# Kernel optimization log

Measured on AMD Instinct MI355X. Metric: run time of the kernel, lower is better.

## Reference

```python
import jax, jax.numpy as jnp
import numpy as np

B, S, H, OUT, L = 32, 4096, 128, 128, 3


def _log_g(x):
    return jnp.where(x >= 0, jnp.log(jax.nn.relu(x) + 0.5), -jax.nn.softplus(-x))


def _cell(x, Wz, bz, Wh, bh):
    # x: [B, S, Din] -> h: [B, S, H]
    k = x @ Wz.T + bz                              # [B,S,H]
    log_z = -jax.nn.softplus(-k)
    log_coeffs = -jax.nn.softplus(k)
    # h_0 = zeros -> log_g(0) = log(0.5)
    log_h0 = jnp.full((x.shape[0], 1, k.shape[-1]), np.log(0.5), dtype=k.dtype)
    log_tilde_h = _log_g(x @ Wh.T + bh)
    log_values = jnp.concatenate([log_h0, log_z + log_tilde_h], axis=1)  # [B,S+1,H]
    # FAITHFUL to source: cumsum over the FEATURE axis (dim=-1), pad along seq
    a_star = jnp.pad(jnp.cumsum(log_coeffs, axis=-1), ((0, 0), (1, 0), (0, 0)))
    log_h = a_star + jax.lax.cumlogsumexp(log_values - a_star, axis=1)
    # torch forward applies sigmoid to the cell output, then drops the h_0 row
    return jax.nn.sigmoid(jnp.exp(log_h))[:, 1:, :]


def setup_inputs() -> dict:
    key = jax.random.key(0)
    ks = jax.random.split(key, 2 * L + 2)
    inp = {"x": jax.random.normal(ks[0], (B, S), dtype=jnp.float32)}
    for l in range(L):
        din = 1 if l == 0 else H
        inp[f"Wz{l}"] = jax.random.normal(ks[1 + 2 * l], (H, din), dtype=jnp.float32) * 0.02
        inp[f"bz{l}"] = jnp.zeros((H,), dtype=jnp.float32)
        inp[f"Wh{l}"] = jax.random.normal(ks[2 + 2 * l], (H, din), dtype=jnp.float32) * 0.02
        inp[f"bh{l}"] = jnp.zeros((H,), dtype=jnp.float32)
    inp["Wout"] = jax.random.normal(ks[-1], (OUT, H * S), dtype=jnp.float32) * (1.0 / np.sqrt(H * S))
    inp["bout"] = jnp.zeros((OUT,), dtype=jnp.float32)
    return inp


def reference(x, Wz0, bz0, Wh0, bh0, Wz1, bz1, Wh1, bh1, Wz2, bz2, Wh2, bh2, Wout, bout):
    h = x[:, :, None]  # [B,S,1]
    for (Wz, bz, Wh, bh) in ((Wz0, bz0, Wh0, bh0), (Wz1, bz1, Wh1, bh1), (Wz2, bz2, Wh2, bh2)):
        h = _cell(h, Wz, bz, Wh, bh)
    flat = h.reshape(h.shape[0], -1)  # [B, S*H]
    return flat @ Wout.T + bout       # [B, OUT]
```

## Files before the change

kernel.cpp:

```cpp
#include <hip/hip_runtime.h>
#include <hip/hip_bf16.h>
#include <math.h>

#define B_   32
#define S_   4096
#define H_   128
#define OUT_ 128
#define P_   (B_*S_)
#define NC_  64
#define CH_  (S_/NC_)
#define NKS_ 512
#define KTOT_ (H_*S_)
#define NEGINF_ (-__builtin_inff())
#define HTP_ 136
#define LOGHALF_ (-0.6931471805599453f)

typedef __bf16 bf16x8 __attribute__((ext_vector_type(8)));
typedef float  f32x4  __attribute__((ext_vector_type(4)));
typedef unsigned short ushort8_t __attribute__((ext_vector_type(8)));

__device__ __forceinline__ float sp_(float x) {
  return __logf(1.f + __expf(x));
}
__device__ __forceinline__ float logg_(float x) {
  float t = (x >= 0.f) ? (x + 0.5f) : __builtin_amdgcn_rcpf(1.f + __expf(-x));
  return __logf(t);
}
__device__ __forceinline__ float lae_(float a, float b) {
  float m = fmaxf(a, b);
  float d = -fabsf(a - b);
  return m + __logf(1.f + __expf(d));
}
__device__ __forceinline__ float sigm_(float e) {
  return __builtin_amdgcn_rcpf(1.f + __expf(-e));
}
__device__ __forceinline__ unsigned short f2bf_(float f) {
  unsigned int u = __float_as_uint(f);
  u += 0x7fffu + ((u >> 16) & 1u);
  return (unsigned short)(u >> 16);
}

#define DPPADD_(v, ctrl, rmask) \
  ((v) + __int_as_float(__builtin_amdgcn_update_dpp( \
      0, __float_as_int(v), (ctrl), (rmask), 0xf, true)))
__device__ __forceinline__ float wscan_(float v) {
  v = DPPADD_(v, 0x111, 0xf);
  v = DPPADD_(v, 0x112, 0xf);
  v = DPPADD_(v, 0x114, 0xf);
  v = DPPADD_(v, 0x118, 0xf);
  v = DPPADD_(v, 0x142, 0xa);
  v = DPPADD_(v, 0x143, 0xc);
  return v;
}


__global__ __launch_bounds__(256) void prep0c_kernel(
    const float* __restrict__ x,
    const float* __restrict__ Wz, const float* __restrict__ bz,
    const float* __restrict__ Wh, const float* __restrict__ bh,
    float* __restrict__ ua, float* __restrict__ tot,
    const float* __restrict__ Wz1, const float* __restrict__ Wh1,
    const float* __restrict__ Wz2, const float* __restrict__ Wh2,
    unsigned short* __restrict__ Wc1, unsigned short* __restrict__ Wc2)
{
  __shared__ float tpart[4][128];
  if (blockIdx.x >= 2048) {
    int idx = (blockIdx.x - 2048) * 256 + threadIdx.x;
    Wc1[idx] = f2bf_(idx < 16384 ? Wz1[idx] : Wh1[idx - 16384]);
    Wc2[idx] = f2bf_(idx < 16384 ? Wz2[idx] : Wh2[idx - 16384]);
    return;
  }
  int lane = threadIdx.x & 63, w = threadIdx.x >> 6;
  float wz0 = Wz[lane], wz1 = Wz[lane + 64];
  float bz0 = bz[lane], bz1 = bz[lane + 64];
  float wh0 = Wh[lane], wh1 = Wh[lane + 64];
  float bh0 = bh[lane], bh1 = bh[lane + 64];
  int blk = blockIdx.x;
  size_t base2 = (size_t)blk * (CH_ * 256);
  int pos0 = blk * CH_;
  float xv[16];
  #pragma unroll
  for (int j = 0; j < 16; ++j) xv[j] = x[pos0 + j * 4 + w];
  float t0 = NEGINF_, t1 = NEGINF_;
  #pragma unroll
  for (int j = 0; j < 16; ++j) {
    int i = j * 4 + w;
    float k0 = fmaf(xv[j], wz0, bz0), k1 = fmaf(xv[j], wz1, bz1);
    float g0 = fmaf(xv[j], wh0, bh0), g1 = fmaf(xv[j], wh1, bh1);
    float lc0 = -sp_(k0), lc1 = -sp_(k1);
    float lv0 = k0 + lc0 + logg_(g0);
    float lv1 = k1 + lc1 + logg_(g1);
    float s0 = wscan_(lc0);
    float c0 = __shfl(s0, 63, 64);
    float s1 = wscan_(lc1) + c0;
    float u0 = lv0 - s0, u1 = lv1 - s1;
    size_t o2 = base2 + (size_t)i * 256;
    *reinterpret_cast<float2*>(&ua[o2 + 2 * lane])       = make_float2(u0, s0);
    *reinterpret_cast<float2*>(&ua[o2 + 128 + 2 * lane]) = make_float2(u1, s1);
    t0 = lae_(t0, u0); t1 = lae_(t1, u1);
  }
  tpart[w][lane] = t0; tpart[w][64 + lane] = t1;
  __syncthreads();
  if (w == 0) {
    int ch = lane;
    tot[(size_t)blk * H_ + ch] =
        lae_(lae_(tpart[0][ch], tpart[1][ch]), lae_(tpart[2][ch], tpart[3][ch]));
    ch = lane + 64;
    tot[(size_t)blk * H_ + ch] =
        lae_(lae_(tpart[0][ch], tpart[1][ch]), lae_(tpart[2][ch], tpart[3][ch]));
  }
}

__global__ __launch_bounds__(256) void kb_kernel(
    const float* __restrict__ totIn,
    const unsigned short* __restrict__ Wc,
    const float* __restrict__ bz, const float* __restrict__ bh,
    float* __restrict__ ua,
    float* __restrict__ totOut)
{
  __shared__ unsigned short hT[64][HTP_];
  __shared__ union {
    float kg[16][260];
    float scr[32][128];
  } ks;
  __shared__ float thand[128];
  __shared__ float tpart[4][128];
  int tid = threadIdx.x;
  int lane = tid & 63, w = tid >> 6;
  int l15 = lane & 15, quad = lane >> 4;
  int half = tid >> 7, ch = tid & 127;
  int blk = blockIdx.x;
  int cidx = blk & (NC_ - 1);
  size_t base2 = (size_t)blk * (CH_ * 256);

  {
    const float* tp = totIn + (size_t)(blk - cidx) * H_ + ch;
    float p0 = NEGINF_, p1 = NEGINF_;
    int i = half;
    for (; i + 2 < cidx; i += 4) {
      float a0 = tp[(size_t)i * H_];
      float a1 = tp[(size_t)(i + 2) * H_];
      p0 = lae_(p0, a0); p1 = lae_(p1, a1);
    }
    for (; i < cidx; i += 2) p0 = lae_(p0, tp[(size_t)i * H_]);
    tpart[half * 2][ch] = p0; tpart[half * 2 + 1][ch] = p1;
  }
  __syncthreads();

  const float* stp = ua + base2 + 2 * ch;

  if (half == 0) {
    float r = LOGHALF_;
    r = lae_(r, tpart[0][ch]); r = lae_(r, tpart[1][ch]);
    r = lae_(r, tpart[2][ch]); r = lae_(r, tpart[3][ch]);
    float uv[32], av[32];
    #pragma unroll
    for (int i = 0; i < 32; ++i) {
      float2 v = *reinterpret_cast<const float2*>(stp + (size_t)i * 256);
      uv[i] = v.x; av[i] = v.y;
    }
    #pragma unroll
    for (int i = 0; i < 32; ++i) {
      r = lae_(r, uv[i]);
      hT[i][ch] = f2bf_(sigm_(__expf(av[i] + r)));
    }
    thand[ch] = r;
  } else {
    float r = NEGINF_;
    float uv[32];
    #pragma unroll
    for (int i = 0; i < 32; ++i)
      uv[i] = stp[(size_t)(32 + i) * 256];
    #pragma unroll
    for (int i = 0; i < 32; ++i) { r = lae_(r, uv[i]); ks.scr[i][ch] = r; }
  }
  __syncthreads();
  if (half == 1) {
    float r31 = thand[ch];
    float av[32];
    #pragma unroll
    for (int i = 0; i < 32; ++i) av[i] = stp[(size_t)(32 + i) * 256 + 1];
    #pragma unroll
    for (int i = 0; i < 32; ++i) {
      float ri = lae_(r31, ks.scr[i][ch]);
      hT[32 + i][ch] = f2bf_(sigm_(__expf(av[i] + ri)));
    }
  }
  __syncthreads();

  float bz0v = bz[lane], bz1v = bz[lane + 64];
  float bh0v = bh[lane], bh1v = bh[lane + 64];
  float t0 = NEGINF_, t1 = NEGINF_;

  for (int t = 0; t < 4; ++t) {
    f32x4 z = {0.f, 0.f, 0.f, 0.f};
    f32x4 acc[4] = {z, z, z, z};
    #pragma unroll
    for (int kk = 0; kk < 4; ++kk) {
      bf16x8 a = *reinterpret_cast<const bf16x8*>(&hT[t * 16 + l15][kk * 32 + quad * 8]);
      #pragma unroll
      for (int nt = 0; nt < 4; ++nt) {
        int n = w * 64 + nt * 16 + l15;
        bf16x8 bf = *reinterpret_cast<const bf16x8*>(Wc + n * 128 + kk * 32 + quad * 8);
        acc[nt] = __builtin_amdgcn_mfma_f32_16x16x32_bf16(a, bf, acc[nt], 0, 0, 0);
      }
    }
    __syncthreads();
    #pragma unroll
    for (int nt = 0; nt < 4; ++nt) {
      int col = w * 64 + nt * 16 + l15;
      #pragma unroll
      for (int r2 = 0; r2 < 4; ++r2)
        ks.kg[quad * 4 + r2][col] = acc[nt][r2];
    }
    __syncthreads();
    #pragma unroll
    for (int i = 0; i < 4; ++i) {
      int row = w + i * 4;
      int sIdx = t * 16 + row;
      float k0 = ks.kg[row][lane]        + bz0v;
      float k1 = ks.kg[row][64 + lane]   + bz1v;
      float g0 = ks.kg[row][128 + lane]  + bh0v;
      float g1 = ks.kg[row][192 + lane]  + bh1v;
      float lc0 = -sp_(k0), lc1 = -sp_(k1);
      float lv0 = k0 + lc0 + logg_(g0);
      float lv1 = k1 + lc1 + logg_(g1);
      float s0 = wscan_(lc0);
      float c0 = __shfl(s0, 63, 64);
      float s1 = wscan_(lc1) + c0;
      float u0 = lv0 - s0, u1 = lv1 - s1;
      size_t o2 = base2 + (size_t)sIdx * 256;
      *reinterpret_cast<float2*>(&ua[o2 + 2 * lane])       = make_float2(u0, s0);
      *reinterpret_cast<float2*>(&ua[o2 + 128 + 2 * lane]) = make_float2(u1, s1);
      t0 = lae_(t0, u0); t1 = lae_(t1, u1);
    }
  }

  tpart[w][lane] = t0; tpart[w][64 + lane] = t1;
  __syncthreads();
  if (w == 0) {
    int c = lane;
    totOut[(size_t)blk * H_ + c] =
        lae_(lae_(tpart[0][c], tpart[1][c]), lae_(tpart[2][c], tpart[3][c]));
    c = lane + 64;
    totOut[(size_t)blk * H_ + c] =
        lae_(lae_(tpart[0][c], tpart[1][c]), lae_(tpart[2][c], tpart[3][c]));
  }
}

__global__ __launch_bounds__(256) void scan3v2_kernel(
    const float* __restrict__ ua,
    const float* __restrict__ totIn, unsigned short* __restrict__ hbf)
{
  __shared__ float scr[32][128];
  __shared__ float thand[128];
  __shared__ float tpart[4][128];
  int tid = threadIdx.x;
  int half = tid >> 7, ch = tid & 127;
  int blk = blockIdx.x;
  int cidx = blk & (NC_ - 1);
  size_t base2 = (size_t)blk * (CH_ * 256);
  size_t baseh = (size_t)blk * (CH_ * H_);
  const float* stp = ua + base2 + 2 * ch;
  unsigned short* hp = hbf + baseh + ch;

  {
    const float* tp = totIn + (size_t)(blk - cidx) * H_ + ch;
    float p0 = NEGINF_, p1 = NEGINF_;
    int i = half;
    for (; i + 2 < cidx; i += 4) {
      float a0 = tp[(size_t)i * H_];
      float a1 = tp[(size_t)(i + 2) * H_];
      p0 = lae_(p0, a0); p1 = lae_(p1, a1);
    }
    for (; i < cidx; i += 2) p0 = lae_(p0, tp[(size_t)i * H_]);
    tpart[half * 2][ch] = p0; tpart[half * 2 + 1][ch] = p1;
  }
  __syncthreads();

  if (half == 0) {
    float r = LOGHALF_;
    r = lae_(r, tpart[0][ch]); r = lae_(r, tpart[1][ch]);
    r = lae_(r, tpart[2][ch]); r = lae_(r, tpart[3][ch]);
    float uv[32], av[32];
    #pragma unroll
    for (int i = 0; i < 32; ++i) {
      float2 v = *reinterpret_cast<const float2*>(stp + (size_t)i * 256);
      uv[i] = v.x; av[i] = v.y;
    }
    #pragma unroll
    for (int i = 0; i < 32; ++i) {
      r = lae_(r, uv[i]);
      hp[(size_t)i * H_] = f2bf_(sigm_(__expf(av[i] + r)));
    }
    thand[ch] = r;
  } else {
    float r = NEGINF_;
    float uv[32];
    #pragma unroll
    for (int i = 0; i < 32; ++i) uv[i] = stp[(size_t)(32 + i) * 256];
    #pragma unroll
    for (int i = 0; i < 32; ++i) { r = lae_(r, uv[i]); scr[i][ch] = r; }
  }
  __syncthreads();
  if (half == 1) {
    float r31 = thand[ch];
    float av[32];
    #pragma unroll
    for (int i = 0; i < 32; ++i) av[i] = stp[(size_t)(32 + i) * 256 + 1];
    #pragma unroll
    for (int i = 0; i < 32; ++i) {
      float ri = lae_(r31, scr[i][ch]);
      hp[(size_t)(32 + i) * H_] = f2bf_(sigm_(__expf(av[i] + ri)));
    }
  }
}

__device__ __forceinline__ void omload_(
    const unsigned short* ap0, const unsigned short* ap1,
    const float* wp0, const float* wp1, int k,
    bf16x8& a0r, bf16x8& a1r, float4 (&wr)[2][2])
{
  a0r = *reinterpret_cast<const bf16x8*>(ap0 + k);
  a1r = *reinterpret_cast<const bf16x8*>(ap1 + k);
  wr[0][0] = *reinterpret_cast<const float4*>(wp0 + k);
  wr[0][1] = *reinterpret_cast<const float4*>(wp0 + k + 4);
  wr[1][0] = *reinterpret_cast<const float4*>(wp1 + k);
  wr[1][1] = *reinterpret_cast<const float4*>(wp1 + k + 4);
}
__device__ __forceinline__ void omstep_(
    const bf16x8& a0r, const bf16x8& a1r,
    const float4 (&wr)[2][2], f32x4 (&acc)[2][2])
{
  #pragma unroll
  for (int nt = 0; nt < 2; ++nt) {
    ushort8_t tt;
    tt[0] = f2bf_(wr[nt][0].x); tt[1] = f2bf_(wr[nt][0].y);
    tt[2] = f2bf_(wr[nt][0].z); tt[3] = f2bf_(wr[nt][0].w);
    tt[4] = f2bf_(wr[nt][1].x); tt[5] = f2bf_(wr[nt][1].y);
    tt[6] = f2bf_(wr[nt][1].z); tt[7] = f2bf_(wr[nt][1].w);
    bf16x8 bf = __builtin_bit_cast(bf16x8, tt);
    acc[0][nt] = __builtin_amdgcn_mfma_f32_16x16x32_bf16(a0r, bf, acc[0][nt], 0, 0, 0);
    acc[1][nt] = __builtin_amdgcn_mfma_f32_16x16x32_bf16(a1r, bf, acc[1][nt], 0, 0, 0);
  }
}

__global__ __launch_bounds__(256) void outmm_kernel(
    const unsigned short* __restrict__ hbf,
    const float* __restrict__ Wout,
    float* __restrict__ part)
{
  const int KSL = KTOT_ / NKS_;
  int tid = threadIdx.x, w = tid >> 6, lane = tid & 63;
  int l15 = lane & 15, quad = lane >> 4;
  int k0base = blockIdx.x * KSL;
  const unsigned short* ap0 = hbf + (size_t)l15 * KTOT_ + k0base + quad * 8;
  const unsigned short* ap1 = hbf + (size_t)(16 + l15) * KTOT_ + k0base + quad * 8;
  const float* wp0 = Wout + (size_t)(w * 32 + l15) * KTOT_ + k0base + quad * 8;
  const float* wp1 = Wout + (size_t)(w * 32 + 16 + l15) * KTOT_ + k0base + quad * 8;
  f32x4 acc[2][2] = {{{0,0,0,0},{0,0,0,0}},{{0,0,0,0},{0,0,0,0}}};
  bf16x8 aA0, aA1, aB0, aB1;
  float4 wvA[2][2], wvB[2][2];
  omload_(ap0, ap1, wp0, wp1, 0, aA0, aA1, wvA);
  for (int ks = 0; ks < KSL; ks += 64) {
    omload_(ap0, ap1, wp0, wp1, ks + 32, aB0, aB1, wvB);
    omstep_(aA0, aA1, wvA, acc);
    if (ks + 64 < KSL) omload_(ap0, ap1, wp0, wp1, ks + 64, aA0, aA1, wvA);
    omstep_(aB0, aB1, wvB, acc);
  }
  float* pp = part + (size_t)blockIdx.x * (B_ * OUT_);
  #pragma unroll
  for (int mt = 0; mt < 2; ++mt)
    #pragma unroll
    for (int nt = 0; nt < 2; ++nt)
      #pragma unroll
      for (int r = 0; r < 4; ++r) {
        int b = mt * 16 + quad * 4 + r;
        int o = w * 32 + nt * 16 + l15;
        pp[b * OUT_ + o] = acc[mt][nt][r];
      }
}

__global__ __launch_bounds__(256) void outred_kernel(
    const float* __restrict__ part, const float* __restrict__ bout,
    float* __restrict__ out)
{
  __shared__ float red[4][64];
  int w = threadIdx.x >> 6, lane = threadIdx.x & 63;
  int idx0 = blockIdx.x * 64;
  float s = 0.f;
  for (int wg = w; wg < NKS_; wg += 4)
    s += part[(size_t)wg * (B_ * OUT_) + idx0 + lane];
  red[w][lane] = s;
  __syncthreads();
  if (w == 0) {
    float r = (red[0][lane] + red[1][lane]) + (red[2][lane] + red[3][lane]);
    int idx = idx0 + lane;
    out[idx] = r + bout[idx & (OUT_ - 1)];
  }
}

extern "C" void kernel_launch(void* const* d_in, const int* in_sizes, int n_in,
                              void* d_out, int out_size, void* d_ws, size_t ws_size,
                              hipStream_t stream)
{
  const float* x    = (const float*)d_in[0];
  const float* Wz[3] = {(const float*)d_in[1], (const float*)d_in[5], (const float*)d_in[9]};
  const float* bz[3] = {(const float*)d_in[2], (const float*)d_in[6], (const float*)d_in[10]};
  const float* Wh[3] = {(const float*)d_in[3], (const float*)d_in[7], (const float*)d_in[11]};
  const float* bh[3] = {(const float*)d_in[4], (const float*)d_in[8], (const float*)d_in[12]};
  const float* Wout = (const float*)d_in[13];
  const float* bout = (const float*)d_in[14];
  float* out = (float*)d_out;

  char* ws = (char*)d_ws;
  float*          ua    = (float*)(ws + 0);
  unsigned short* hbf   = (unsigned short*)(ws + 134217728);
  unsigned short* Wc1   = (unsigned short*)(ws + 167772160);
  unsigned short* Wc2   = (unsigned short*)(ws + 167837696);
  float*          totA  = (float*)(ws + 167903232);
  float*          totB  = (float*)(ws + 168951808);
  float*          part  = (float*)(ws + 170000384);

  prep0c_kernel<<<B_ * NC_ + 128, 256, 0, stream>>>(
      x, Wz[0], bz[0], Wh[0], bh[0], ua, totA,
      Wz[1], Wh[1], Wz[2], Wh[2], Wc1, Wc2);

  kb_kernel<<<B_ * NC_, 256, 0, stream>>>(totA, Wc1, bz[1], bh[1], ua, totB);
  kb_kernel<<<B_ * NC_, 256, 0, stream>>>(totB, Wc2, bz[2], bh[2], ua, totA);

  scan3v2_kernel<<<B_ * NC_, 256, 0, stream>>>(ua, totA, hbf);

  outmm_kernel<<<NKS_, 256, 0, stream>>>(hbf, Wout, part);
  outred_kernel<<<(B_ * OUT_) / 64, 256, 0, stream>>>(part, bout, out);
}
```

Before: 670.9 us.

## Fuse layer scans into one cooperative kernel with grid syncs

Merges the two kb_kernel launches and the final scan kernel into a single cooperative kernel of 1024 blocks, each handling two chunks, with grid.sync between layers. It also splits the 32-step register arrays into 16-step blocks, which lowers register pressure enough to meet a launch bound of 4 blocks per CU. The aim is to remove launch gaps and tail effects between dependent kernels. In exchange each layer now ends in a grid-wide barrier, each block processes its two chunks one after the other, and the per-block scan work is serial. The old three-kernel path stays as a fallback.

```diff
diff --git a/kernel.cpp b/kernel.cpp
--- a/kernel.cpp
+++ b/kernel.cpp
@@ -1,4 +1,5 @@
 #include <hip/hip_runtime.h>
+#include <hip/hip_cooperative_groups.h>
 #include <hip/hip_bf16.h>
 #include <math.h>
 
@@ -14,6 +15,8 @@
 #define NEGINF_ (-__builtin_inff())
 #define HTP_ 136
 #define LOGHALF_ (-0.6931471805599453f)
+
+namespace cg = cooperative_groups;
 
 typedef __bf16 bf16x8 __attribute__((ext_vector_type(8)));
 typedef float  f32x4  __attribute__((ext_vector_type(4)));
@@ -111,25 +114,16 @@
   }
 }
 
-__global__ __launch_bounds__(256) void kb_kernel(
-    const float* __restrict__ totIn,
-    const unsigned short* __restrict__ Wc,
+__device__ __forceinline__ void kb_body(
+    const float* __restrict__ totIn, const unsigned short* __restrict__ Wc,
     const float* __restrict__ bz, const float* __restrict__ bh,
-    float* __restrict__ ua,
-    float* __restrict__ totOut)
-{
-  __shared__ unsigned short hT[64][HTP_];
-  __shared__ union {
-    float kg[16][260];
-    float scr[32][128];
-  } ks;
-  __shared__ float thand[128];
-  __shared__ float tpart[4][128];
+    float* __restrict__ ua, float* __restrict__ totOut, int blk,
+    unsigned short (*hT)[HTP_], float* ksu, float* thand, float (*tpart)[128])
+{
   int tid = threadIdx.x;
   int lane = tid & 63, w = tid >> 6;
   int l15 = lane & 15, quad = lane >> 4;
   int half = tid >> 7, ch = tid & 127;
-  int blk = blockIdx.x;
   int cidx = blk & (NC_ - 1);
   size_t base2 = (size_t)blk * (CH_ * 256);
 
@@ -153,37 +147,42 @@
     float r = LOGHALF_;
     r = lae_(r, tpart[0][ch]); r = lae_(r, tpart[1][ch]);
     r = lae_(r, tpart[2][ch]); r = lae_(r, tpart[3][ch]);
-    float uv[32], av[32];
-    #pragma unroll
-    for (int i = 0; i < 32; ++i) {
-      float2 v = *reinterpret_cast<const float2*>(stp + (size_t)i * 256);
-      uv[i] = v.x; av[i] = v.y;
-    }
-    #pragma unroll
-    for (int i = 0; i < 32; ++i) {
-      r = lae_(r, uv[i]);
-      hT[i][ch] = f2bf_(sigm_(__expf(av[i] + r)));
+    for (int i0 = 0; i0 < 32; i0 += 16) {
+      float uv[16], av[16];
+      #pragma unroll
+      for (int i = 0; i < 16; ++i) {
+        float2 v = *reinterpret_cast<const float2*>(stp + (size_t)(i0 + i) * 256);
+        uv[i] = v.x; av[i] = v.y;
+      }
+      #pragma unroll
+      for (int i = 0; i < 16; ++i) {
+        r = lae_(r, uv[i]);
+        hT[i0 + i][ch] = f2bf_(sigm_(__expf(av[i] + r)));
+      }
     }
     thand[ch] = r;
   } else {
     float r = NEGINF_;
-    float uv[32];
-    #pragma unroll
-    for (int i = 0; i < 32; ++i)
-      uv[i] = stp[(size_t)(32 + i) * 256];
-    #pragma unroll
-    for (int i = 0; i < 32; ++i) { r = lae_(r, uv[i]); ks.scr[i][ch] = r; }
+    for (int i0 = 0; i0 < 32; i0 += 16) {
+      float uv[16];
+      #pragma unroll
+      for (int i = 0; i < 16; ++i) uv[i] = stp[(size_t)(32 + i0 + i) * 256];
+      #pragma unroll
+      for (int i = 0; i < 16; ++i) { r = lae_(r, uv[i]); ksu[(i0 + i) * 128 + ch] = r; }
+    }
   }
   __syncthreads();
   if (half == 1) {
     float r31 = thand[ch];
-    float av[32];
-    #pragma unroll
-    for (int i = 0; i < 32; ++i) av[i] = stp[(size_t)(32 + i) * 256 + 1];
-    #pragma unroll
-    for (int i = 0; i < 32; ++i) {
-      float ri = lae_(r31, ks.scr[i][ch]);
-      hT[32 + i][ch] = f2bf_(sigm_(__expf(av[i] + ri)));
+    for (int i0 = 0; i0 < 32; i0 += 16) {
+      float av[16];
+      #pragma unroll
+      for (int i = 0; i < 16; ++i) av[i] = stp[(size_t)(32 + i0 + i) * 256 + 1];
+      #pragma unroll
+      for (int i = 0; i < 16; ++i) {
+        float ri = lae_(r31, ksu[(i0 + i) * 128 + ch]);
+        hT[32 + i0 + i][ch] = f2bf_(sigm_(__expf(av[i] + ri)));
+      }
     }
   }
   __syncthreads();
@@ -201,8 +200,8 @@
       #pragma unroll
       for (int nt = 0; nt < 4; ++nt) {
         int n = w * 64 + nt * 16 + l15;
-        bf16x8 bf = *reinterpret_cast<const bf16x8*>(Wc + n * 128 + kk * 32 + quad * 8);
-        acc[nt] = __builtin_amdgcn_mfma_f32_16x16x32_bf16(a, bf, acc[nt], 0, 0, 0);
+        bf16x8 bfv = *reinterpret_cast<const bf16x8*>(Wc + n * 128 + kk * 32 + quad * 8);
+        acc[nt] = __builtin_amdgcn_mfma_f32_16x16x32_bf16(a, bfv, acc[nt], 0, 0, 0);
       }
     }
     __syncthreads();
@@ -211,17 +210,17 @@
       int col = w * 64 + nt * 16 + l15;
       #pragma unroll
       for (int r2 = 0; r2 < 4; ++r2)
-        ks.kg[quad * 4 + r2][col] = acc[nt][r2];
+        ksu[(quad * 4 + r2) * 260 + col] = acc[nt][r2];
     }
     __syncthreads();
     #pragma unroll
     for (int i = 0; i < 4; ++i) {
       int row = w + i * 4;
       int sIdx = t * 16 + row;
-      float k0 = ks.kg[row][lane]        + bz0v;
-      float k1 = ks.kg[row][64 + lane]   + bz1v;
-      float g0 = ks.kg[row][128 + lane]  + bh0v;
-      float g1 = ks.kg[row][192 + lane]  + bh1v;
+      float k0 = ksu[row * 260 + lane]        + bz0v;
+      float k1 = ksu[row * 260 + 64 + lane]   + bz1v;
+      float g0 = ksu[row * 260 + 128 + lane]  + bh0v;
+      float g1 = ksu[row * 260 + 192 + lane]  + bh1v;
       float lc0 = -sp_(k0), lc1 = -sp_(k1);
       float lv0 = k0 + lc0 + logg_(g0);
       float lv1 = k1 + lc1 + logg_(g1);
@@ -248,16 +247,13 @@
   }
 }
 
-__global__ __launch_bounds__(256) void scan3v2_kernel(
-    const float* __restrict__ ua,
-    const float* __restrict__ totIn, unsigned short* __restrict__ hbf)
-{
-  __shared__ float scr[32][128];
-  __shared__ float thand[128];
-  __shared__ float tpart[4][128];
+__device__ __forceinline__ void scan3_body(
+    const float* __restrict__ ua, const float* __restrict__ totIn,
+    unsigned short* __restrict__ hbf, int blk,
+    float* scr, float* thand, float (*tpart)[128])
+{
   int tid = threadIdx.x;
   int half = tid >> 7, ch = tid & 127;
-  int blk = blockIdx.x;
   int cidx = blk & (NC_ - 1);
   size_t base2 = (size_t)blk * (CH_ * 256);
   size_t baseh = (size_t)blk * (CH_ * H_);
@@ -282,38 +278,99 @@
     float r = LOGHALF_;
     r = lae_(r, tpart[0][ch]); r = lae_(r, tpart[1][ch]);
     r = lae_(r, tpart[2][ch]); r = lae_(r, tpart[3][ch]);
-    float uv[32], av[32];
-    #pragma unroll
-    for (int i = 0; i < 32; ++i) {
-      float2 v = *reinterpret_cast<const float2*>(stp + (size_t)i * 256);
-      uv[i] = v.x; av[i] = v.y;
-    }
-    #pragma unroll
-    for (int i = 0; i < 32; ++i) {
-      r = lae_(r, uv[i]);
-      hp[(size_t)i * H_] = f2bf_(sigm_(__expf(av[i] + r)));
+    for (int i0 = 0; i0 < 32; i0 += 16) {
+      float uv[16], av[16];
+      #pragma unroll
+      for (int i = 0; i < 16; ++i) {
+        float2 v = *reinterpret_cast<const float2*>(stp + (size_t)(i0 + i) * 256);
+        uv[i] = v.x; av[i] = v.y;
+      }
+      #pragma unroll
+      for (int i = 0; i < 16; ++i) {
+        r = lae_(r, uv[i]);
+        hp[(size_t)(i0 + i) * H_] = f2bf_(sigm_(__expf(av[i] + r)));
+      }
     }
     thand[ch] = r;
   } else {
     float r = NEGINF_;
-    float uv[32];
-    #pragma unroll
-    for (int i = 0; i < 32; ++i) uv[i] = stp[(size_t)(32 + i) * 256];
-    #pragma unroll
-    for (int i = 0; i < 32; ++i) { r = lae_(r, uv[i]); scr[i][ch] = r; }
+    for (int i0 = 0; i0 < 32; i0 += 16) {
+      float uv[16];
+      #pragma unroll
+      for (int i = 0; i < 16; ++i) uv[i] = stp[(size_t)(32 + i0 + i) * 256];
+      #pragma unroll
+      for (int i = 0; i < 16; ++i) { r = lae_(r, uv[i]); scr[(i0 + i) * 128 + ch] = r; }
+    }
   }
   __syncthreads();
   if (half == 1) {
     float r31 = thand[ch];
-    float av[32];
-    #pragma unroll
-    for (int i = 0; i < 32; ++i) av[i] = stp[(size_t)(32 + i) * 256 + 1];
-    #pragma unroll
-    for (int i = 0; i < 32; ++i) {
-      float ri = lae_(r31, scr[i][ch]);
-      hp[(size_t)(32 + i) * H_] = f2bf_(sigm_(__expf(av[i] + ri)));
-    }
-  }
+    for (int i0 = 0; i0 < 32; i0 += 16) {
+      float av[16];
+      #pragma unroll
+      for (int i = 0; i < 16; ++i) av[i] = stp[(size_t)(32 + i0 + i) * 256 + 1];
+      #pragma unroll
+      for (int i = 0; i < 16; ++i) {
+        float ri = lae_(r31, scr[(i0 + i) * 128 + ch]);
+        hp[(size_t)(32 + i0 + i) * H_] = f2bf_(sigm_(__expf(av[i] + ri)));
+      }
+    }
+  }
+}
+
+__global__ __launch_bounds__(256, 4) void scans_kernel(
+    const float* __restrict__ tot0,
+    const unsigned short* __restrict__ Wc1,
+    const float* __restrict__ bz1, const float* __restrict__ bh1,
+    const unsigned short* __restrict__ Wc2,
+    const float* __restrict__ bz2, const float* __restrict__ bh2,
+    float* __restrict__ ua, float* __restrict__ tot1, float* __restrict__ tot2,
+    unsigned short* __restrict__ hbf)
+{
+  __shared__ unsigned short hT[64][HTP_];
+  __shared__ float ksu[16 * 260];
+  __shared__ float thand[128];
+  __shared__ float tpart[4][128];
+  cg::grid_group grid = cg::this_grid();
+  int b2 = blockIdx.x * 2;
+
+  kb_body(tot0, Wc1, bz1, bh1, ua, tot1, b2,     hT, ksu, thand, tpart);
+  __syncthreads();
+  kb_body(tot0, Wc1, bz1, bh1, ua, tot1, b2 + 1, hT, ksu, thand, tpart);
+  __threadfence();
+  grid.sync();
+
+  kb_body(tot1, Wc2, bz2, bh2, ua, tot2, b2,     hT, ksu, thand, tpart);
+  __syncthreads();
+  kb_body(tot1, Wc2, bz2, bh2, ua, tot2, b2 + 1, hT, ksu, thand, tpart);
+  __threadfence();
+  grid.sync();
+
+  scan3_body(ua, tot2, hbf, b2,     ksu, thand, tpart);
+  __syncthreads();
+  scan3_body(ua, tot2, hbf, b2 + 1, ksu, thand, tpart);
+}
+
+__global__ __launch_bounds__(256) void kb_kernel(
+    const float* __restrict__ totIn, const unsigned short* __restrict__ Wc,
+    const float* __restrict__ bz, const float* __restrict__ bh,
+    float* __restrict__ ua, float* __restrict__ totOut)
+{
+  __shared__ unsigned short hT[64][HTP_];
+  __shared__ float ksu[16 * 260];
+  __shared__ float thand[128];
+  __shared__ float tpart[4][128];
+  kb_body(totIn, Wc, bz, bh, ua, totOut, blockIdx.x, hT, ksu, thand, tpart);
+}
+
+__global__ __launch_bounds__(256) void scan3v2_kernel(
+    const float* __restrict__ ua, const float* __restrict__ totIn,
+    unsigned short* __restrict__ hbf)
+{
+  __shared__ float scr[32 * 128];
+  __shared__ float thand[128];
+  __shared__ float tpart[4][128];
+  scan3_body(ua, totIn, hbf, blockIdx.x, scr, thand, tpart);
 }
 
 __device__ __forceinline__ void omload_(
@@ -339,9 +396,9 @@
     tt[2] = f2bf_(wr[nt][0].z); tt[3] = f2bf_(wr[nt][0].w);
     tt[4] = f2bf_(wr[nt][1].x); tt[5] = f2bf_(wr[nt][1].y);
     tt[6] = f2bf_(wr[nt][1].z); tt[7] = f2bf_(wr[nt][1].w);
-    bf16x8 bf = __builtin_bit_cast(bf16x8, tt);
-    acc[0][nt] = __builtin_amdgcn_mfma_f32_16x16x32_bf16(a0r, bf, acc[0][nt], 0, 0, 0);
-    acc[1][nt] = __builtin_amdgcn_mfma_f32_16x16x32_bf16(a1r, bf, acc[1][nt], 0, 0, 0);
+    bf16x8 bfv = __builtin_bit_cast(bf16x8, tt);
+    acc[0][nt] = __builtin_amdgcn_mfma_f32_16x16x32_bf16(a0r, bfv, acc[0][nt], 0, 0, 0);
+    acc[1][nt] = __builtin_amdgcn_mfma_f32_16x16x32_bf16(a1r, bfv, acc[1][nt], 0, 0, 0);
   }
 }
 
@@ -420,16 +477,39 @@
   unsigned short* Wc2   = (unsigned short*)(ws + 167837696);
   float*          totA  = (float*)(ws + 167903232);
   float*          totB  = (float*)(ws + 168951808);
-  float*          part  = (float*)(ws + 170000384);
+  float*          totC  = (float*)(ws + 170000384);
+  float*          part  = (float*)(ws + 171048960);
 
   prep0c_kernel<<<B_ * NC_ + 128, 256, 0, stream>>>(
       x, Wz[0], bz[0], Wh[0], bh[0], ua, totA,
       Wz[1], Wh[1], Wz[2], Wh[2], Wc1, Wc2);
 
-  kb_kernel<<<B_ * NC_, 256, 0, stream>>>(totA, Wc1, bz[1], bh[1], ua, totB);
-  kb_kernel<<<B_ * NC_, 256, 0, stream>>>(totB, Wc2, bz[2], bh[2], ua, totA);
-
-  scan3v2_kernel<<<B_ * NC_, 256, 0, stream>>>(ua, totA, hbf);
+  int coop = 0;
+  {
+    int maxb = 0;
+    if (hipOccupancyMaxActiveBlocksPerMultiprocessor(
+            &maxb, (const void*)scans_kernel, 256, 0) == hipSuccess &&
+        maxb >= 4) {
+      const float* tot0p = totA;
+      const unsigned short* wc1p = Wc1;
+      const float* bz1p = bz[1]; const float* bh1p = bh[1];
+      const unsigned short* wc2p = Wc2;
+      const float* bz2p = bz[2]; const float* bh2p = bh[2];
+      float* uap = ua; float* t1p = totB; float* t2p = totC;
+      unsigned short* hbfp = hbf;
+      void* kargs[] = {(void*)&tot0p, (void*)&wc1p, (void*)&bz1p, (void*)&bh1p,
+                       (void*)&wc2p, (void*)&bz2p, (void*)&bh2p,
+                       (void*)&uap, (void*)&t1p, (void*)&t2p, (void*)&hbfp};
+      if (hipLaunchCooperativeKernel((const void*)scans_kernel, dim3(1024),
+                                     dim3(256), kargs, 0, stream) == hipSuccess)
+        coop = 1;
+    }
+  }
+  if (!coop) {
+    kb_kernel<<<B_ * NC_, 256, 0, stream>>>(totA, Wc1, bz[1], bh[1], ua, totB);
+    kb_kernel<<<B_ * NC_, 256, 0, stream>>>(totB, Wc2, bz[2], bh[2], ua, totC);
+    scan3v2_kernel<<<B_ * NC_, 256, 0, stream>>>(ua, totC, hbf);
+  }
 
   outmm_kernel<<<NKS_, 256, 0, stream>>>(hbf, Wout, part);
   outred_kernel<<<(B_ * OUT_) / 64, 256, 0, stream>>>(part, bout, out);
```

After: 682.1 us. About the same (+1.7%).
